# Performance work log

Hardware: AMD Instinct MI355X
Metric: run time of the kernel (lower is better)

Reference implementation:

```python
import jax, jax.numpy as jnp
import numpy as np

D_MODEL = 32; D_STATE = 16; D_CONV = 4; D_INNER = 64; DT_RANK = 2
BATCH = 64; C_IN = 64; PATCH = 32; FEATURE_DIM = 128


def setup_inputs() -> dict:
    key = jax.random.key(0)
    ks = jax.random.split(key, 14)
    def w(k, shape, fan_in):
        return jax.random.normal(k, shape, jnp.float32) * np.float32(1.0 / np.sqrt(fan_in))
    dt_init = jnp.exp(jax.random.uniform(ks[12], (D_INNER,), jnp.float32,
                                         np.float32(np.log(1e-3)), np.float32(np.log(1e-1))))
    return {
        "x": jax.random.normal(ks[0], (BATCH, C_IN, PATCH, PATCH), jnp.float32),
        "conv_w": w(ks[1], (D_MODEL, C_IN), C_IN),
        "conv_b": jnp.zeros((D_MODEL,), jnp.float32),
        "bn_gamma": jnp.ones((D_MODEL,), jnp.float32),
        "bn_beta": jnp.zeros((D_MODEL,), jnp.float32),
        "bn_mean": jnp.zeros((D_MODEL,), jnp.float32),
        "bn_var": jnp.ones((D_MODEL,), jnp.float32),
        "in_proj_w": w(ks[2], (2 * D_INNER, D_MODEL), D_MODEL),
        "conv1d_w": w(ks[3], (D_INNER, D_CONV), D_CONV),
        "conv1d_b": jnp.zeros((D_INNER,), jnp.float32),
        "x_proj_w": w(ks[4], (DT_RANK + 2 * D_STATE, D_INNER), D_INNER),
        "dt_proj_w": w(ks[5], (D_INNER, DT_RANK), DT_RANK),
        "dt_proj_b": jnp.log(jnp.expm1(dt_init)),
        "A_log": jnp.log(jnp.tile(jnp.arange(1, D_STATE + 1, dtype=jnp.float32), (D_INNER, 1))),
        "D_param": jnp.ones((D_INNER,), jnp.float32),
        "out_proj_w": w(ks[6], (D_MODEL, D_INNER), D_INNER),
        "fc_w": w(ks[7], (FEATURE_DIM, D_MODEL), D_MODEL),
        "fc_b": jnp.zeros((FEATURE_DIM,), jnp.float32),
    }


def reference(x, conv_w, conv_b, bn_gamma, bn_beta, bn_mean, bn_var, in_proj_w,
              conv1d_w, conv1d_b, x_proj_w, dt_proj_w, dt_proj_b, A_log, D_param,
              out_proj_w, fc_w, fc_b):
    Bsz = x.shape[0]
    # --- stem: 1x1 conv + BatchNorm (eval stats) + exact GELU ---
    h = jnp.einsum('bchw,dc->bdhw', x, conv_w) + conv_b[:, None, None]
    scale = bn_gamma / jnp.sqrt(bn_var + 1e-5)
    h = (h - bn_mean[:, None, None]) * scale[:, None, None] + bn_beta[:, None, None]
    h = jax.nn.gelu(h, approximate=False)
    u = h.reshape(Bsz, D_MODEL, -1).transpose(0, 2, 1)   # [B, L, d_model], L = H*W
    # --- Mamba block ---
    xz = u @ in_proj_w.T                                  # [B, L, 2*d_inner]
    xm, z = xz[..., :D_INNER], xz[..., D_INNER:]
    # depthwise causal conv1d over the sequence
    xt = jnp.pad(xm.transpose(0, 2, 1), ((0, 0), (0, 0), (D_CONV - 1, 0)))
    xt = jax.lax.conv_general_dilated(xt, conv1d_w[:, None, :], (1,), 'VALID',
                                      feature_group_count=D_INNER,
                                      dimension_numbers=('NCH', 'OIH', 'NCH'))
    xm = jax.nn.silu(xt + conv1d_b[None, :, None]).transpose(0, 2, 1)  # [B, L, d_inner]
    x_dbl = xm @ x_proj_w.T                               # [B, L, dt_rank + 2*d_state]
    dt = jax.nn.softplus(x_dbl[..., :DT_RANK] @ dt_proj_w.T + dt_proj_b)  # [B, L, d_inner]
    Bt = x_dbl[..., DT_RANK:DT_RANK + D_STATE]            # [B, L, d_state]
    Ct = x_dbl[..., DT_RANK + D_STATE:]                   # [B, L, d_state]
    A = -jnp.exp(A_log)                                   # [d_inner, d_state]

    def step(hst, inp):
        u_t, dt_t, B_t, C_t = inp                         # [B,d],[B,d],[B,n],[B,n]
        hst = jnp.exp(dt_t[:, :, None] * A) * hst + (dt_t * u_t)[:, :, None] * B_t[:, None, :]
        return hst, jnp.einsum('bdn,bn->bd', hst, C_t)

    h0 = jnp.zeros((Bsz, D_INNER, D_STATE), xm.dtype)
    _, ys = jax.lax.scan(step, h0, (xm.transpose(1, 0, 2), dt.transpose(1, 0, 2),
                                    Bt.transpose(1, 0, 2), Ct.transpose(1, 0, 2)))
    y = ys.transpose(1, 0, 2) + xm * D_param
    y = y * jax.nn.silu(z)
    out = y @ out_proj_w.T                                # [B, L, d_model]
    pooled = out.mean(axis=1)                             # [B, d_model]
    return pooled @ fc_w.T + fc_b                         # [B, FEATURE_DIM]
```

## Files before the change

### kernel.cpp

```cpp
#include <hip/hip_runtime.h>
#include <hip/hip_bf16.h>
#include <math.h>

#define L 1024
typedef __hip_bfloat16 bf;
typedef __attribute__((ext_vector_type(8))) short short8v;
typedef __attribute__((ext_vector_type(4))) short short4v;

__device__ __forceinline__ float b2f(bf v) { return __bfloat162float(v); }
__device__ __forceinline__ bf f2b(float v) { return __float2bfloat16(v); }
__device__ __forceinline__ float bits2f(short s) {
  union { unsigned u; float f; } cv; cv.u = ((unsigned)(unsigned short)s) << 16; return cv.f;
}
union Pack4 { short4v v; unsigned short e[4]; };
union Pack8 { short8v v; unsigned short e[8]; };
__device__ __forceinline__ unsigned short f2bits(float v) {
  union { bf b; unsigned short u; } cv; cv.b = __float2bfloat16(v); return cv.u;
}

__global__ __launch_bounds__(256, 2) void k_front(
    const float* __restrict__ x, const float* __restrict__ conv_w,
    const float* __restrict__ conv_b, const float* __restrict__ gamma,
    const float* __restrict__ beta, const float* __restrict__ mean,
    const float* __restrict__ var, const float* __restrict__ ipw,
    bf* __restrict__ xm, bf* __restrict__ z) {
  __shared__ float xs[64 * 65];
  __shared__ float hsh[64][34];
  int t = threadIdx.x;
  int b = blockIdx.x >> 4;
  int l0 = (blockIdx.x & 15) << 6;
  const float* xg = x + (size_t)b * 65536 + l0;
#pragma unroll
  for (int k = 0; k < 16; ++k) {
    int i = t + k * 256;
    int c = i >> 6, ll = i & 63;
    xs[c * 65 + ll] = xg[(size_t)c * L + ll];
  }
  __syncthreads();
  int lq = t & 63;
  int q = __builtin_amdgcn_readfirstlane(t >> 6);
  int l = l0 | lq;
  float hacc[8];
#pragma unroll
  for (int dd = 0; dd < 8; ++dd) hacc[dd] = conv_b[q * 8 + dd];
#pragma unroll
  for (int c4 = 0; c4 < 16; ++c4) {
    float x0 = xs[(c4 * 4 + 0) * 65 + lq];
    float x1 = xs[(c4 * 4 + 1) * 65 + lq];
    float x2 = xs[(c4 * 4 + 2) * 65 + lq];
    float x3 = xs[(c4 * 4 + 3) * 65 + lq];
#pragma unroll
    for (int dd = 0; dd < 8; ++dd) {
      const float* w = conv_w + (q * 8 + dd) * 64 + c4 * 4;
      hacc[dd] = fmaf(x0, w[0], fmaf(x1, w[1],
                 fmaf(x2, w[2], fmaf(x3, w[3], hacc[dd]))));
    }
  }
#pragma unroll
  for (int dd = 0; dd < 8; ++dd) {
    int d = q * 8 + dd;
    float sc = gamma[d] * rsqrtf(var[d] + 1e-5f);
    float acc = (hacc[dd] - mean[d]) * sc + beta[d];
    hsh[lq][d] = 0.5f * acc * (1.0f + erff(acc * 0.70710678118654752f));
  }
  __syncthreads();
  float h[32];
#pragma unroll
  for (int d = 0; d < 32; ++d) h[d] = hsh[lq][d];
  if (q < 2) {
    short8v* xr8 = (short8v*)(xm + ((size_t)b * 1024 + l) * 64) + q * 4;
#pragma unroll
    for (int j8 = 0; j8 < 4; ++j8) {
      Pack8 p;
#pragma unroll
      for (int e = 0; e < 8; ++e) {
        int j = q * 32 + j8 * 8 + e;
        float acc = 0.f;
#pragma unroll
        for (int d = 0; d < 32; ++d) acc = fmaf(h[d], ipw[j * 32 + d], acc);
        p.e[e] = f2bits(acc);
      }
      xr8[j8] = p.v;
    }
  } else {
    bf* zp = z + (size_t)b * 65536 + l;
#pragma unroll
    for (int jj = 0; jj < 32; ++jj) {
      int j = (q - 2) * 32 + jj;
      float acc = 0.f;
#pragma unroll
      for (int d = 0; d < 32; ++d) acc = fmaf(h[d], ipw[(j + 64) * 32 + d], acc);
      zp[(size_t)j * L] = f2b(acc);
    }
  }
}

__global__ __launch_bounds__(256, 2) void k_mid(
    const bf* __restrict__ xm, const float* __restrict__ c1w,
    const float* __restrict__ c1b, const float* __restrict__ xpw,
    const float* __restrict__ dtw, const float* __restrict__ dtbp,
    bf* __restrict__ u, bf* __restrict__ dt_o,
    bf* __restrict__ Bt, bf* __restrict__ Ct) {
  __shared__ bf    xsh[67 * 68];
  __shared__ float wsh[34 * 64];
  __shared__ float ush[64 * 65];
  __shared__ float xdh[64 * 35];
  int t = threadIdx.x;
  int lq = t & 63;
  int q = __builtin_amdgcn_readfirstlane(t >> 6);
  int b = blockIdx.x >> 4;
  int l0 = (blockIdx.x & 15) << 6;
  int l = l0 | lq;
  {
    const short4v* xg4 = (const short4v*)(xm + ((size_t)b * 1024 + l0 - 3) * 64);
    for (int i = t; i < 1072; i += 256) {
      int r = i >> 4, c4 = i & 15;
      short4v v;
      if (l0 == 0 && r < 3) { v[0] = v[1] = v[2] = v[3] = 0; }
      else v = xg4[i];
      *(short4v*)(&xsh[r * 68 + c4 * 4]) = v;
    }
    const float4* wg = (const float4*)xpw;
    float4* ws4 = (float4*)wsh;
    for (int i = t; i < 544; i += 256) ws4[i] = wg[i];
  }
  __syncthreads();
  float um[16];
#pragma unroll
  for (int dd = 0; dd < 16; ++dd) um[dd] = c1b[q * 16 + dd];
#pragma unroll
  for (int k = 0; k < 4; ++k) {
    const short4v* xr = (const short4v*)(&xsh[(lq + k) * 68 + q * 16]);
#pragma unroll
    for (int c4 = 0; c4 < 4; ++c4) {
      short4v v = xr[c4];
#pragma unroll
      for (int e = 0; e < 4; ++e)
        um[c4 * 4 + e] = fmaf(c1w[(q * 16 + c4 * 4 + e) * 4 + k],
                              bits2f(v[e]), um[c4 * 4 + e]);
    }
  }
  {
    bf* up = u + (size_t)b * 65536 + l;
#pragma unroll
    for (int dd = 0; dd < 16; ++dd) {
      float s = um[dd];
      s = s / (1.f + __expf(-s));
      ush[lq * 65 + q * 16 + dd] = s;
      up[(size_t)(q * 16 + dd) * L] = f2b(s);
    }
  }
  __syncthreads();
  {
    float um64[64];
#pragma unroll
    for (int d = 0; d < 64; ++d) um64[d] = ush[lq * 65 + d];
    int k0 = (q < 2) ? q * 9 : 18 + (q - 2) * 8;
    int nk = (q < 2) ? 9 : 8;
    for (int kk = 0; kk < nk; ++kk) {
      int k = k0 + kk;
      const float4* wr = (const float4*)(&wsh[k * 64]);
      float acc = 0.f;
#pragma unroll
      for (int d4 = 0; d4 < 16; ++d4) {
        float4 w4 = wr[d4];
        acc = fmaf(um64[d4 * 4 + 0], w4.x, fmaf(um64[d4 * 4 + 1], w4.y,
              fmaf(um64[d4 * 4 + 2], w4.z, fmaf(um64[d4 * 4 + 3], w4.w, acc))));
      }
      xdh[lq * 35 + k] = acc;
    }
  }
  __syncthreads();
  {
    float xd0 = xdh[lq * 35 + 0], xd1 = xdh[lq * 35 + 1];
    bf* dp = dt_o + (size_t)b * 65536 + l;
#pragma unroll
    for (int dd = 0; dd < 16; ++dd) {
      int d = q * 16 + dd;
      float raw = fmaf(xd0, dtw[d * 2], fmaf(xd1, dtw[d * 2 + 1], dtbp[d]));
      float sp = fmaxf(raw, 0.f) + log1pf(__expf(-fabsf(raw)));
      dp[(size_t)d * L] = f2b(sp);
    }
    int i = l & 31, c = l >> 5;
    size_t basei = ((size_t)b * 16384 + (size_t)i * 128 + c * 4) >> 2;
    short4v* B4 = (short4v*)Bt;
    short4v* C4 = (short4v*)Ct;
    Pack4 pb, pc;
#pragma unroll
    for (int nn = 0; nn < 4; ++nn) {
      pb.e[nn] = f2bits(xdh[lq * 35 + 2 + q * 4 + nn]);
      pc.e[nn] = f2bits(xdh[lq * 35 + 18 + q * 4 + nn]);
    }
    B4[basei + (size_t)q * 1024] = pb.v;
    C4[basei + (size_t)q * 1024] = pc.v;
  }
}

__global__ __launch_bounds__(256, 2) void k_scan(
    const bf* __restrict__ u, const bf* __restrict__ dt,
    const bf* __restrict__ z, const bf* __restrict__ Bt,
    const bf* __restrict__ Ct, const float* __restrict__ A_log,
    const float* __restrict__ Dp, float* __restrict__ pooled64) {
  __shared__ bf Bsh[16384];
  __shared__ bf Csh[16384];
  int phys = blockIdx.x;
  int b = phys & 63;
  int dgrp = phys >> 6;
  int t = threadIdx.x;
  int d_local = t >> 5, c = t & 31;
  int d = dgrp * 8 + d_local;
  int g = b * 64 + d;

  {
    const short8v* Bg8 = (const short8v*)(Bt + (size_t)b * 16384);
    const short8v* Cg8 = (const short8v*)(Ct + (size_t)b * 16384);
    short8v* Bs8 = (short8v*)Bsh;
    short8v* Cs8 = (short8v*)Csh;
#pragma unroll
    for (int q = 0; q < 8; ++q) {
      Bs8[t + q * 256] = Bg8[t + q * 256];
      Cs8[t + q * 256] = Cg8[t + q * 256];
    }
  }
  __syncthreads();

  float An[16];
#pragma unroll
  for (int n = 0; n < 16; ++n) An[n] = -__expf(A_log[d * 16 + n]);
  const short4v* dps = (const short4v*)(dt + (size_t)g * L + c * 32);
  const short4v* ups = (const short4v*)(u  + (size_t)g * L + c * 32);
  const short4v* zps = (const short4v*)(z  + (size_t)g * L + c * 32);
  const short4v* Bs4 = (const short4v*)Bsh;
  const short4v* Cs4 = (const short4v*)Csh;
  float Dd = Dp[d];

  float h[16], pi[16], q[16];
#pragma unroll
  for (int n = 0; n < 16; ++n) { h[n] = 0.f; pi[n] = 1.f; q[n] = 0.f; }
  float base = 0.f;

#pragma unroll 1
  for (int t4 = 0; t4 < 8; ++t4) {
    short4v d4 = dps[t4], u4 = ups[t4], z4 = zps[t4];
#pragma unroll
    for (int i = 0; i < 4; ++i) {
      int step = t4 * 4 + i;
      float dtv = bits2f(d4[i]);
      float uv  = bits2f(u4[i]);
      float zv  = bits2f(z4[i]);
      float sv  = zv / (1.f + __expf(-zv));
      float du  = dtv * uv;
      int slot = step * 32 + c;
      float y0 = 0.f, y1 = 0.f;
#pragma unroll
      for (int n4 = 0; n4 < 4; ++n4) {
        short4v bq = Bs4[n4 * 1024 + slot];
        short4v cq = Cs4[n4 * 1024 + slot];
#pragma unroll
        for (int nn = 0; nn < 4; ++nn) {
          int n = n4 * 4 + nn;
          float a = __expf(dtv * An[n]);
          float Bv = bits2f(bq[nn]);
          float Cv = bits2f(cq[nn]);
          h[n] = fmaf(a, h[n], du * Bv);
          pi[n] *= a;
          if (nn & 1) y1 = fmaf(h[n], Cv, y1); else y0 = fmaf(h[n], Cv, y0);
          q[n] = fmaf(sv * pi[n], Cv, q[n]);
        }
      }
      base = fmaf(sv, (y0 + y1) + uv * Dd, base);
    }
  }

#pragma unroll
  for (int s = 1; s < 32; s <<= 1) {
    bool act = (c >= s);
#pragma unroll
    for (int n = 0; n < 16; ++n) {
      float Po = __shfl_up(pi[n], (unsigned)s, 32);
      float Oo = __shfl_up(h[n], (unsigned)s, 32);
      if (act) { h[n] = fmaf(pi[n], Oo, h[n]); pi[n] *= Po; }
    }
  }
  float pooled = base;
#pragma unroll
  for (int n = 0; n < 16; ++n) {
    float v = __shfl_up(h[n], 1u, 32);
    float hin = (c == 0) ? 0.f : v;
    pooled = fmaf(q[n], hin, pooled);
  }
#pragma unroll
  for (int s = 1; s < 32; s <<= 1) pooled += __shfl_xor(pooled, s, 32);
  if (c == 0) pooled64[g] = pooled;
}

__global__ __launch_bounds__(128) void k_fc(
    const float* __restrict__ pooled64, const float* __restrict__ opw,
    const float* __restrict__ fcw, const float* __restrict__ fcb,
    float* __restrict__ out) {
  __shared__ float p64[64];
  __shared__ float o32[32];
  int b = blockIdx.x, t = threadIdx.x;
  if (t < 64) p64[t] = pooled64[b * 64 + t];
  __syncthreads();
  if (t < 32) {
    float s = 0.f;
#pragma unroll
    for (int d0 = 0; d0 < 64; ++d0) s = fmaf(p64[d0], opw[t * 64 + d0], s);
    o32[t] = s * (1.f / 1024.f);
  }
  __syncthreads();
  float acc = fcb[t];
#pragma unroll
  for (int j = 0; j < 32; ++j) acc = fmaf(o32[j], fcw[t * 32 + j], acc);
  out[b * 128 + t] = acc;
}

extern "C" void kernel_launch(void* const* d_in, const int* in_sizes, int n_in,
                              void* d_out, int out_size, void* d_ws, size_t ws_size,
                              hipStream_t stream) {
  const float* x      = (const float*)d_in[0];
  const float* conv_w = (const float*)d_in[1];
  const float* conv_b = (const float*)d_in[2];
  const float* bn_g   = (const float*)d_in[3];
  const float* bn_b   = (const float*)d_in[4];
  const float* bn_m   = (const float*)d_in[5];
  const float* bn_v   = (const float*)d_in[6];
  const float* ipw    = (const float*)d_in[7];
  const float* c1w    = (const float*)d_in[8];
  const float* c1b    = (const float*)d_in[9];
  const float* xpw    = (const float*)d_in[10];
  const float* dtw    = (const float*)d_in[11];
  const float* dtbp   = (const float*)d_in[12];
  const float* A_log  = (const float*)d_in[13];
  const float* Dp     = (const float*)d_in[14];
  const float* opw    = (const float*)d_in[15];
  const float* fcw    = (const float*)d_in[16];
  const float* fcb    = (const float*)d_in[17];

  char* ws = (char*)d_ws;
  bf* xmb = (bf*)(ws + 0);
  bf* zb  = (bf*)(ws + 8388608);
  bf* ub  = (bf*)(ws + 16777216);
  bf* dtb = (bf*)(ws + 25165824);
  bf* Btb = (bf*)(ws + 33554432);
  bf* Ctb = (bf*)(ws + 35651584);
  float* pooled = (float*)(ws + 37748736);

  hipLaunchKernelGGL(k_front, dim3(1024), dim3(256), 0, stream,
                     x, conv_w, conv_b, bn_g, bn_b, bn_m, bn_v, ipw, xmb, zb);
  hipLaunchKernelGGL(k_mid, dim3(1024), dim3(256), 0, stream,
                     xmb, c1w, c1b, xpw, dtw, dtbp, ub, dtb, Btb, Ctb);
  hipLaunchKernelGGL(k_scan, dim3(512), dim3(256), 0, stream,
                     ub, dtb, zb, Btb, Ctb, A_log, Dp, pooled);
  hipLaunchKernelGGL(k_fc, dim3(64), dim3(128), 0, stream,
                     pooled, opw, fcw, fcb, (float*)d_out);
}
```

Measured before the change: 109.6 us.

## Split scan state across lane pairs and read B/C directly from global memory

The scan kernel now assigns each d channel to a full 64-lane wavefront, with adjacent lanes each owning half of the 16 state dimensions. This halves per-thread registers and doubles the grid to 1024 blocks. The per-block LDS staging of B and C, and the barrier that went with it, are removed, so B/C are loaded straight from global memory through the cache. In exchange, dt/u/z loads and the exp/silu work are duplicated across each lane pair, and B/C traffic now depends on cache hits rather than shared memory.

Result: no change. 110.7 us (+1.0%).

```diff
diff --git a/kernel.cpp b/kernel.cpp
--- a/kernel.cpp
+++ b/kernel.cpp
@@ -201,42 +201,30 @@
     const bf* __restrict__ z, const bf* __restrict__ Bt,
     const bf* __restrict__ Ct, const float* __restrict__ A_log,
     const float* __restrict__ Dp, float* __restrict__ pooled64) {
-  __shared__ bf Bsh[16384];
-  __shared__ bf Csh[16384];
   int phys = blockIdx.x;
   int b = phys & 63;
   int dgrp = phys >> 6;
   int t = threadIdx.x;
-  int d_local = t >> 5, c = t & 31;
-  int d = dgrp * 8 + d_local;
+  int q = __builtin_amdgcn_readfirstlane(t >> 6);
+  int lane = t & 63;
+  int c = lane >> 1;
+  int nh = lane & 1;
+  int d = dgrp * 4 + q;
   int g = b * 64 + d;
 
-  {
-    const short8v* Bg8 = (const short8v*)(Bt + (size_t)b * 16384);
-    const short8v* Cg8 = (const short8v*)(Ct + (size_t)b * 16384);
-    short8v* Bs8 = (short8v*)Bsh;
-    short8v* Cs8 = (short8v*)Csh;
-#pragma unroll
-    for (int q = 0; q < 8; ++q) {
-      Bs8[t + q * 256] = Bg8[t + q * 256];
-      Cs8[t + q * 256] = Cg8[t + q * 256];
-    }
-  }
-  __syncthreads();
-
-  float An[16];
-#pragma unroll
-  for (int n = 0; n < 16; ++n) An[n] = -__expf(A_log[d * 16 + n]);
+  float An[8];
+#pragma unroll
+  for (int n = 0; n < 8; ++n) An[n] = -__expf(A_log[d * 16 + nh * 8 + n]);
   const short4v* dps = (const short4v*)(dt + (size_t)g * L + c * 32);
   const short4v* ups = (const short4v*)(u  + (size_t)g * L + c * 32);
   const short4v* zps = (const short4v*)(z  + (size_t)g * L + c * 32);
-  const short4v* Bs4 = (const short4v*)Bsh;
-  const short4v* Cs4 = (const short4v*)Csh;
+  const short4v* B4 = (const short4v*)(Bt + (size_t)b * 16384);
+  const short4v* C4 = (const short4v*)(Ct + (size_t)b * 16384);
   float Dd = Dp[d];
 
-  float h[16], pi[16], q[16];
-#pragma unroll
-  for (int n = 0; n < 16; ++n) { h[n] = 0.f; pi[n] = 1.f; q[n] = 0.f; }
+  float h[8], pi[8], qa[8];
+#pragma unroll
+  for (int n = 0; n < 8; ++n) { h[n] = 0.f; pi[n] = 1.f; qa[n] = 0.f; }
   float base = 0.f;
 
 #pragma unroll 1
@@ -251,24 +239,28 @@
       float sv  = zv / (1.f + __expf(-zv));
       float du  = dtv * uv;
       int slot = step * 32 + c;
+      short4v bq0 = B4[(nh * 2 + 0) * 1024 + slot];
+      short4v bq1 = B4[(nh * 2 + 1) * 1024 + slot];
+      short4v cq0 = C4[(nh * 2 + 0) * 1024 + slot];
+      short4v cq1 = C4[(nh * 2 + 1) * 1024 + slot];
       float y0 = 0.f, y1 = 0.f;
 #pragma unroll
-      for (int n4 = 0; n4 < 4; ++n4) {
-        short4v bq = Bs4[n4 * 1024 + slot];
-        short4v cq = Cs4[n4 * 1024 + slot];
-#pragma unroll
-        for (int nn = 0; nn < 4; ++nn) {
-          int n = n4 * 4 + nn;
-          float a = __expf(dtv * An[n]);
-          float Bv = bits2f(bq[nn]);
-          float Cv = bits2f(cq[nn]);
-          h[n] = fmaf(a, h[n], du * Bv);
-          pi[n] *= a;
-          if (nn & 1) y1 = fmaf(h[n], Cv, y1); else y0 = fmaf(h[n], Cv, y0);
-          q[n] = fmaf(sv * pi[n], Cv, q[n]);
-        }
+      for (int e = 0; e < 4; ++e) {
+        float a0 = __expf(dtv * An[e]);
+        h[e] = fmaf(a0, h[e], du * bits2f(bq0[e]));
+        pi[e] *= a0;
+        float Cv0 = bits2f(cq0[e]);
+        y0 = fmaf(h[e], Cv0, y0);
+        qa[e] = fmaf(sv * pi[e], Cv0, qa[e]);
+        float a1 = __expf(dtv * An[4 + e]);
+        h[4 + e] = fmaf(a1, h[4 + e], du * bits2f(bq1[e]));
+        pi[4 + e] *= a1;
+        float Cv1 = bits2f(cq1[e]);
+        y1 = fmaf(h[4 + e], Cv1, y1);
+        qa[4 + e] = fmaf(sv * pi[4 + e], Cv1, qa[4 + e]);
       }
-      base = fmaf(sv, (y0 + y1) + uv * Dd, base);
+      float dterm = nh ? 0.f : uv * Dd;
+      base = fmaf(sv, (y0 + y1) + dterm, base);
     }
   }
 
@@ -276,22 +268,22 @@
   for (int s = 1; s < 32; s <<= 1) {
     bool act = (c >= s);
 #pragma unroll
-    for (int n = 0; n < 16; ++n) {
-      float Po = __shfl_up(pi[n], (unsigned)s, 32);
-      float Oo = __shfl_up(h[n], (unsigned)s, 32);
+    for (int n = 0; n < 8; ++n) {
+      float Po = __shfl_up(pi[n], (unsigned)(2 * s));
+      float Oo = __shfl_up(h[n], (unsigned)(2 * s));
       if (act) { h[n] = fmaf(pi[n], Oo, h[n]); pi[n] *= Po; }
     }
   }
   float pooled = base;
 #pragma unroll
-  for (int n = 0; n < 16; ++n) {
-    float v = __shfl_up(h[n], 1u, 32);
+  for (int n = 0; n < 8; ++n) {
+    float v = __shfl_up(h[n], 2u);
     float hin = (c == 0) ? 0.f : v;
-    pooled = fmaf(q[n], hin, pooled);
-  }
-#pragma unroll
-  for (int s = 1; s < 32; s <<= 1) pooled += __shfl_xor(pooled, s, 32);
-  if (c == 0) pooled64[g] = pooled;
+    pooled = fmaf(qa[n], hin, pooled);
+  }
+#pragma unroll
+  for (int s = 1; s < 64; s <<= 1) pooled += __shfl_xor(pooled, s);
+  if (lane == 0) pooled64[g] = pooled;
 }
 
 __global__ __launch_bounds__(128) void k_fc(
@@ -351,7 +343,7 @@
                      x, conv_w, conv_b, bn_g, bn_b, bn_m, bn_v, ipw, xmb, zb);
   hipLaunchKernelGGL(k_mid, dim3(1024), dim3(256), 0, stream,
                      xmb, c1w, c1b, xpw, dtw, dtbp, ub, dtb, Btb, Ctb);
-  hipLaunchKernelGGL(k_scan, dim3(512), dim3(256), 0, stream,
+  hipLaunchKernelGGL(k_scan, dim3(1024), dim3(256), 0, stream,
                      ub, dtb, zb, Btb, Ctb, A_log, Dp, pooled);
   hipLaunchKernelGGL(k_fc, dim3(64), dim3(128), 0, stream,
                      pooled, opw, fcw, fcb, (float*)d_out);
```
